# Optimization experiments

Measured on AMD Instinct MI355X. Metric: run time of the kernel, lower is better.

## Reference

```python
import jax, jax.numpy as jnp
import numpy as np

NUM_Q_HEADS = 32
NUM_KV_HEADS = 8
GROUP = NUM_Q_HEADS // NUM_KV_HEADS  # 4, matches hardcoded repeat_interleave(repeats=4)
HEAD_DIM = 128
ROPE_BASE = 10000.0


def _rope_cos_sin(seq_len, head_dim, dtype):
    # [S, D/2] angle tables for rotate-half RoPE
    inv_freq = 1.0 / (ROPE_BASE ** (jnp.arange(0, head_dim, 2, dtype=jnp.float32) / head_dim))
    ang = jnp.arange(seq_len, dtype=jnp.float32)[:, None] * inv_freq[None, :]
    return jnp.cos(ang).astype(dtype), jnp.sin(ang).astype(dtype)


def _apply_rope(x, cos, sin):
    # x: [B, S, H, D]; cos/sin: [S, D/2] broadcast over batch & heads
    x1, x2 = jnp.split(x, 2, axis=-1)
    c = cos[None, :, None, :]
    s = sin[None, :, None, :]
    return jnp.concatenate([x1 * c - x2 * s, x2 * c + x1 * s], axis=-1)


def setup_inputs() -> dict:
    key = jax.random.key(0)
    k1, k2, k3 = jax.random.split(key, 3)
    B, S, E = 2, 2048, 4096
    x = jax.random.normal(k1, (B, S, E), dtype=jnp.float32)
    w_in = jax.random.normal(k2, (6144, E), dtype=jnp.float32) * 0.02   # torch Linear weight [out, in]
    w_out = jax.random.normal(k3, (E, E), dtype=jnp.float32) * 0.02
    return {"x": x, "w_in": w_in, "w_out": w_out}


def reference(x, w_in, w_out):
    B, S, E = x.shape
    D = HEAD_DIM
    qkv = jnp.einsum('bse,fe->bsf', x, w_in)  # [B, S, 6144]
    parts = jnp.split(qkv, GROUP + 2, axis=-1)  # 6 equal chunks of width E//GROUP
    q = jnp.concatenate(parts[:GROUP], axis=-1).reshape(B, S, NUM_Q_HEADS, D)
    k = parts[GROUP].reshape(B, S, NUM_KV_HEADS, D)
    v = parts[GROUP + 1].reshape(B, S, NUM_KV_HEADS, D)

    cos, sin = _rope_cos_sin(S, D, x.dtype)
    q = _apply_rope(q, cos, sin)
    k = _apply_rope(k, cos, sin)

    # GQA without materializing repeated K/V: group q heads by kv head.
    # repeat_interleave(k, 4, dim=2) maps q head h -> kv head h // 4, i.e. q view [B,S,HKV,G,D]
    qg = q.reshape(B, S, NUM_KV_HEADS, GROUP, D)
    scale = 1.0 / jnp.sqrt(jnp.asarray(D, dtype=x.dtype))
    scores = jnp.einsum('bqhgd,bkhd->bhgqk', qg, k) * scale  # [B, HKV, G, S, S]
    causal = jnp.tril(jnp.ones((S, S), dtype=bool))
    scores = jnp.where(causal[None, None, None, :, :], scores, jnp.asarray(-1e30, dtype=scores.dtype))
    probs = jax.nn.softmax(scores, axis=-1)
    out = jnp.einsum('bhgqk,bkhd->bqhgd', probs, v)  # [B, S, HKV, G, D]
    out = out.reshape(B, S, E)
    return jnp.einsum('bse,fe->bsf', out, w_out)
```

## Files before the change

kernel.cpp:

```cpp
#include <hip/hip_runtime.h>
#include <hip/hip_bf16.h>
#include <stdint.h>

typedef unsigned short u16;
typedef __bf16 bf16x8 __attribute__((ext_vector_type(8)));
typedef u16 u16x8 __attribute__((ext_vector_type(8)));
typedef float f32x4 __attribute__((ext_vector_type(4)));
typedef float f32x16 __attribute__((ext_vector_type(16)));
typedef uint32_t u32x4 __attribute__((ext_vector_type(4)));

#define DEV __device__ __forceinline__
#define SBAR() asm volatile("s_barrier" ::: "memory")
#define SCHEDB() __builtin_amdgcn_sched_barrier(0)

DEV u16 f2bf(float f) {
  uint32_t u = __builtin_bit_cast(uint32_t, f);
  return (u16)((u + 0x7FFFu + ((u >> 16) & 1u)) >> 16);
}
DEV float bf2f(u16 h) { return __builtin_bit_cast(float, (uint32_t)h << 16); }

DEV void gload_lds16(const void* g, void* l) {
  __builtin_amdgcn_global_load_lds((const __attribute__((address_space(1))) uint32_t*)g,
                                   (__attribute__((address_space(3))) uint32_t*)l, 16, 0, 0);
}

DEV uint32_t cvtpk(float lo, float hi) {
  uint32_t r;
  asm("v_cvt_pk_bf16_f32 %0, %1, %2" : "=v"(r) : "v"(lo), "v"(hi));
  return r;
}
DEV void plswap(uint32_t& a, uint32_t& b) {
  asm("v_permlane32_swap_b32 %0, %1" : "+v"(a), "+v"(b));
}

DEV void cvt8(const float* __restrict__ in, u16* __restrict__ out, int i) {
  const float4* p = reinterpret_cast<const float4*>(in + i);
  float4 a = p[0], b = p[1];
  u16x8 o;
  o[0] = f2bf(a.x); o[1] = f2bf(a.y); o[2] = f2bf(a.z); o[3] = f2bf(a.w);
  o[4] = f2bf(b.x); o[5] = f2bf(b.y); o[6] = f2bf(b.z); o[7] = f2bf(b.w);
  *reinterpret_cast<u16x8*>(out + i) = o;
}

__global__ void prep_all(const float* __restrict__ x, const float* __restrict__ w_in,
                         const float* __restrict__ w_out, u16* __restrict__ xb,
                         u16* __restrict__ wib, u16* __restrict__ wob,
                         float* __restrict__ ct, float* __restrict__ st) {
  int b = blockIdx.x;
  if (b < 8192) {
    cvt8(x, xb, (b * 256 + threadIdx.x) * 8);
  } else if (b < 20480) {
    cvt8(w_in, wib, ((b - 8192) * 256 + threadIdx.x) * 8);
  } else if (b < 28672) {
    cvt8(w_out, wob, ((b - 20480) * 256 + threadIdx.x) * 8);
  } else {
    int i = (b - 28672) * 256 + threadIdx.x;
    int s = i >> 6, d = i & 63;
    float invf = powf(10000.0f, -(float)d * (1.0f / 64.0f));
    float ang = (float)s * invf;
    ct[i] = cosf(ang);
    st[i] = sinf(ang);
  }
}

__global__ void rope_and_vt(u16* __restrict__ qkv, const float* __restrict__ ct,
                            const float* __restrict__ st, u16* __restrict__ vtg) {
  const int tid = threadIdx.x;
  if (blockIdx.x < 5120) {
    int idx = blockIdx.x * 256 + tid;
    int grp = idx & 7;
    int head = (idx >> 3) % 40;
    int row = idx / 320;
    int s = row & 2047;
    size_t f0 = head < 32 ? (size_t)head * 128 : (size_t)4096 + (size_t)(head - 32) * 128;
    u16* p = qkv + (size_t)row * 6144 + f0 + grp * 8;
    u16x8 a = *reinterpret_cast<const u16x8*>(p);
    u16x8 b = *reinterpret_cast<const u16x8*>(p + 64);
    const float4* cp = reinterpret_cast<const float4*>(ct + s * 64 + grp * 8);
    const float4* sp = reinterpret_cast<const float4*>(st + s * 64 + grp * 8);
    float4 c0 = cp[0], c1 = cp[1], s0 = sp[0], s1 = sp[1];
    float cc[8] = {c0.x, c0.y, c0.z, c0.w, c1.x, c1.y, c1.z, c1.w};
    float ss[8] = {s0.x, s0.y, s0.z, s0.w, s1.x, s1.y, s1.z, s1.w};
    u16x8 o1, o2;
#pragma unroll
    for (int i = 0; i < 8; i++) {
      float x1 = bf2f(a[i]), x2 = bf2f(b[i]);
      o1[i] = f2bf(x1 * cc[i] - x2 * ss[i]);
      o2[i] = f2bf(x2 * cc[i] + x1 * ss[i]);
    }
    *reinterpret_cast<u16x8*>(p) = o1;
    *reinterpret_cast<u16x8*>(p + 64) = o2;
  } else {
    int id = blockIdx.x - 5120;
    int j = id & 31, kvh = (id >> 5) & 7, b = id >> 8;
    const size_t rowB = (size_t)b * 2048;
    u16* img = vtg + (size_t)id * 8192;
#pragma unroll
    for (int p = 0; p < 4; p++) {
      int lin = p * 256 + tid;
      int d = lin >> 3, c = lin & 7;
      const u16* src = qkv + (rowB + j * 64 + c * 8) * 6144 + 5120 + kvh * 128 + d;
      u16x8 v;
#pragma unroll
      for (int i = 0; i < 8; i++) v[i] = src[(size_t)i * 6144];
      *reinterpret_cast<u16x8*>(img + d * 64 + ((c ^ (d & 7)) << 3)) = v;
    }
  }
}

DEV void store_c(float* C, size_t idx, float v) { C[idx] = v; }
DEV void store_c(u16* C, size_t idx, float v) { C[idx] = f2bf(v); }

template <typename OutT>
__global__ __launch_bounds__(512, 2) void gemm256(const u16* __restrict__ A, const u16* __restrict__ B,
                                                  OutT* __restrict__ C, int M, int N, int K, int ldc) {
  __shared__ __align__(16) u16 lds[65536];
  char* LB = (char*)lds;
  const int tid = threadIdx.x;
  const int w = tid >> 6, lane = tid & 63;
  const int l15 = lane & 15, l4 = lane >> 4;
  const int wm = w >> 2, wn = w & 3;

  int nwg = gridDim.x;
  int q = nwg >> 3, rr = nwg & 7;
  int xcd = blockIdx.x & 7, idx = blockIdx.x >> 3;
  int sw = (xcd < rr ? xcd * (q + 1) : rr * (q + 1) + (xcd - rr) * q) + idx;
  int gxn = N >> 8;
  int by = sw / gxn, bx = sw - by * gxn;
  const int row0 = by << 8, col0 = bx << 8;
  const int NT = K >> 6;

  const int srow = w * 8 + (lane >> 3);
  const int sc16 = (lane & 7) ^ ((lane >> 3) & 7);
  const u16* gA = A + (size_t)(row0 + srow) * K + sc16 * 8;
  const u16* gB = B + (size_t)(col0 + srow) * K + sc16 * 8;

  const int fl = (l15 & 7) << 4;
  const int aoff = (wm * 128 + l15) * 128 + l4 * 16;
  const int boff = (wn * 64 + l15) * 128 + l4 * 16;

  f32x4 acc[8][4] = {};
  bf16x8 fA[4][2], fB0[2][2], fBc[2][2];

#define STAGE_A(kt, h, base)                                                      \
  {                                                                               \
    const u16* g_ = gA + (size_t)((h)*128) * K + (size_t)(kt)*64;                 \
    gload_lds16(g_, (base) + (h)*16384 + w * 1024);                               \
    gload_lds16(g_ + (size_t)64 * K, (base) + (h)*16384 + 8192 + w * 1024);       \
  }
#define STAGE_B(kt, h, base)                                                      \
  {                                                                               \
    const u16* g_ = gB + (size_t)((h)*128) * K + (size_t)(kt)*64;                 \
    gload_lds16(g_, (base) + (h)*16384 + w * 1024);                               \
    gload_lds16(g_ + (size_t)64 * K, (base) + (h)*16384 + 8192 + w * 1024);       \
  }
#define MFMA_Q(FB, MH, NH)                                                        \
  _Pragma("unroll") for (int kk = 0; kk < 2; kk++) {                              \
    _Pragma("unroll") for (int mf = 0; mf < 4; mf++) {                            \
      _Pragma("unroll") for (int nf = 0; nf < 2; nf++) {                          \
        acc[(MH)*4 + mf][(NH)*2 + nf] = __builtin_amdgcn_mfma_f32_16x16x32_bf16(  \
            fA[mf][kk], FB[nf][kk], acc[(MH)*4 + mf][(NH)*2 + nf], 0, 0, 0);      \
      }                                                                           \
    }                                                                             \
  }

  STAGE_A(0, 0, LB);
  STAGE_A(0, 1, LB);
  STAGE_B(0, 0, LB + 65536);
  STAGE_B(0, 1, LB + 65536);
  STAGE_A(1, 0, LB + 32768);
  STAGE_B(1, 0, LB + 98304);
  STAGE_B(1, 1, LB + 98304);
  asm volatile("s_waitcnt vmcnt(6)" ::: "memory");
  SBAR();

  for (int t = 0; t < NT; ++t) {
    char* ac = LB + (t & 1) * 32768;
    char* bc = LB + 65536 + (t & 1) * 32768;
    char* an = LB + ((t + 1) & 1) * 32768;

    if (t + 1 < NT) STAGE_A(t + 1, 1, an);

#pragma unroll
    for (int mf = 0; mf < 4; mf++)
#pragma unroll
      for (int kk = 0; kk < 2; kk++)
        fA[mf][kk] = *(const bf16x8*)(ac + ((aoff + mf * 2048 + kk * 64) ^ fl));
    SCHEDB();
#pragma unroll
    for (int nf = 0; nf < 2; nf++)
#pragma unroll
      for (int kk = 0; kk < 2; kk++)
        fB0[nf][kk] = *(const bf16x8*)(bc + ((boff + nf * 2048 + kk * 64) ^ fl));
    SCHEDB();
#pragma unroll
    for (int nf = 0; nf < 2; nf++)
#pragma unroll
      for (int kk = 0; kk < 2; kk++)
        fBc[nf][kk] = *(const bf16x8*)(bc + ((boff + (nf + 2) * 2048 + kk * 64) ^ fl));
    SCHEDB();

    asm volatile("s_waitcnt lgkmcnt(4)" ::: "memory");
    SCHEDB();
    __builtin_amdgcn_s_setprio(1);
    MFMA_Q(fB0, 0, 0);
    __builtin_amdgcn_s_setprio(0);

    asm volatile("s_waitcnt lgkmcnt(0)" ::: "memory");
    SCHEDB();
    __builtin_amdgcn_s_setprio(1);
    MFMA_Q(fBc, 0, 1);
    __builtin_amdgcn_s_setprio(0);

#pragma unroll
    for (int mf = 0; mf < 4; mf++)
#pragma unroll
      for (int kk = 0; kk < 2; kk++)
        fA[mf][kk] = *(const bf16x8*)(ac + ((aoff + (mf + 4) * 2048 + kk * 64) ^ fl));
    asm volatile("s_waitcnt lgkmcnt(0)" ::: "memory");
    SCHEDB();

    SBAR();
    if (t + 2 < NT) {
      STAGE_B(t + 2, 0, bc);
      STAGE_B(t + 2, 1, bc);
      STAGE_A(t + 2, 0, ac);
    }
    __builtin_amdgcn_s_setprio(1);
    MFMA_Q(fBc, 1, 1);
    MFMA_Q(fB0, 1, 0);
    __builtin_amdgcn_s_setprio(0);

    if (t + 2 < NT) {
      asm volatile("s_waitcnt vmcnt(6)" ::: "memory");
      SBAR();
    } else if (t + 1 < NT) {
      asm volatile("s_waitcnt vmcnt(0)" ::: "memory");
      SBAR();
    }
  }

#pragma unroll
  for (int mf = 0; mf < 8; mf++)
#pragma unroll
    for (int nf = 0; nf < 4; nf++)
#pragma unroll
      for (int r = 0; r < 4; r++) {
        size_t row = (size_t)row0 + wm * 128 + mf * 16 + l4 * 4 + r;
        size_t col = (size_t)col0 + wn * 64 + nf * 16 + l15;
        store_c(C, row * (size_t)ldc + col, acc[mf][nf][r]);
      }
#undef STAGE_A
#undef STAGE_B
#undef MFMA_Q
}

__global__ __launch_bounds__(512, 2) void gemm_bn128(const u16* __restrict__ A, const u16* __restrict__ B,
                                                     u16* __restrict__ C, int M, int N, int K, int ldc) {
  __shared__ __align__(16) u16 lds[49152];
  char* LB = (char*)lds;
  const int tid = threadIdx.x;
  const int w = tid >> 6, lane = tid & 63;
  const int l15 = lane & 15, l4 = lane >> 4;
  const int wm = w >> 2, wn = w & 3;

  int nwg = gridDim.x;
  int q = nwg >> 3, rr = nwg & 7;
  int xcd = blockIdx.x & 7, idx = blockIdx.x >> 3;
  int sw = (xcd < rr ? xcd * (q + 1) : rr * (q + 1) + (xcd - rr) * q) + idx;
  int gxn = N >> 7;
  int by = sw / gxn, bx = sw - by * gxn;
  const int row0 = by << 8, col0 = bx << 7;
  const int NT = K >> 6;

  const int srow = w * 8 + (lane >> 3);
  const int sc16 = (lane & 7) ^ ((lane >> 3) & 7);
  const u16* gA = A + (size_t)(row0 + srow) * K + sc16 * 8;
  const u16* gB = B + (size_t)(col0 + srow) * K + sc16 * 8;

  const int fl = (l15 & 7) << 4;
  const int aoff = (wm * 128 + l15) * 128 + l4 * 16;
  const int boff = (wn * 32 + l15) * 128 + l4 * 16;

  f32x4 acc[8][2] = {};
  bf16x8 fA[4][2], fB[2][2];

#define STAGE_A(kt, h, base)                                                      \
  {                                                                               \
    const u16* g_ = gA + (size_t)((h)*128) * K + (size_t)(kt)*64;                 \
    gload_lds16(g_, (base) + (h)*16384 + w * 1024);                               \
    gload_lds16(g_ + (size_t)64 * K, (base) + (h)*16384 + 8192 + w * 1024);       \
  }
#define STAGE_B(kt, base)                                                         \
  {                                                                               \
    const u16* g_ = gB + (size_t)(kt)*64;                                         \
    gload_lds16(g_, (base) + w * 1024);                                           \
    gload_lds16(g_ + (size_t)64 * K, (base) + 8192 + w * 1024);                   \
  }

  STAGE_A(0, 0, LB);
  STAGE_A(0, 1, LB);
  STAGE_B(0, LB + 65536);
  STAGE_A(1, 0, LB + 32768);
  STAGE_B(1, LB + 65536 + 16384);
  asm volatile("s_waitcnt vmcnt(4)" ::: "memory");
  SBAR();

  for (int t = 0; t < NT; ++t) {
    char* ac = LB + (t & 1) * 32768;
    char* bc = LB + 65536 + (t & 1) * 16384;
    char* an = LB + ((t + 1) & 1) * 32768;

    if (t + 1 < NT) STAGE_A(t + 1, 1, an);

#pragma unroll
    for (int mf = 0; mf < 4; mf++)
#pragma unroll
      for (int kk = 0; kk < 2; kk++)
        fA[mf][kk] = *(const bf16x8*)(ac + ((aoff + mf * 2048 + kk * 64) ^ fl));
#pragma unroll
    for (int nf = 0; nf < 2; nf++)
#pragma unroll
      for (int kk = 0; kk < 2; kk++)
        fB[nf][kk] = *(const bf16x8*)(bc + ((boff + nf * 2048 + kk * 64) ^ fl));
    SCHEDB();
    asm volatile("s_waitcnt lgkmcnt(0)" ::: "memory");
    SCHEDB();
    __builtin_amdgcn_s_setprio(1);
#pragma unroll
    for (int kk = 0; kk < 2; kk++)
#pragma unroll
      for (int mf = 0; mf < 4; mf++)
#pragma unroll
        for (int nf = 0; nf < 2; nf++)
          acc[mf][nf] = __builtin_amdgcn_mfma_f32_16x16x32_bf16(fA[mf][kk], fB[nf][kk], acc[mf][nf], 0, 0, 0);
    __builtin_amdgcn_s_setprio(0);

#pragma unroll
    for (int mf = 0; mf < 4; mf++)
#pragma unroll
      for (int kk = 0; kk < 2; kk++)
        fA[mf][kk] = *(const bf16x8*)(ac + ((aoff + (mf + 4) * 2048 + kk * 64) ^ fl));
    asm volatile("s_waitcnt lgkmcnt(0)" ::: "memory");
    SCHEDB();

    SBAR();
    if (t + 2 < NT) {
      STAGE_A(t + 2, 0, ac);
      STAGE_B(t + 2, bc);
    }
    __builtin_amdgcn_s_setprio(1);
#pragma unroll
    for (int kk = 0; kk < 2; kk++)
#pragma unroll
      for (int mf = 0; mf < 4; mf++)
#pragma unroll
        for (int nf = 0; nf < 2; nf++)
          acc[mf + 4][nf] = __builtin_amdgcn_mfma_f32_16x16x32_bf16(fA[mf][kk], fB[nf][kk], acc[mf + 4][nf], 0, 0, 0);
    __builtin_amdgcn_s_setprio(0);

    if (t + 2 < NT) {
      asm volatile("s_waitcnt vmcnt(4)" ::: "memory");
      SBAR();
    } else if (t + 1 < NT) {
      asm volatile("s_waitcnt vmcnt(0)" ::: "memory");
      SBAR();
    }
  }

#pragma unroll
  for (int mf = 0; mf < 8; mf++)
#pragma unroll
    for (int nf = 0; nf < 2; nf++)
#pragma unroll
      for (int r = 0; r < 4; r++) {
        size_t row = (size_t)row0 + wm * 128 + mf * 16 + l4 * 4 + r;
        size_t col = (size_t)col0 + wn * 32 + nf * 16 + l15;
        C[row * (size_t)ldc + col] = f2bf(acc[mf][nf][r]);
      }
#undef STAGE_A
#undef STAGE_B
}

__global__ __launch_bounds__(256, 2) void attn_fwd(const u16* __restrict__ qkv,
                                                   const u16* __restrict__ vtg,
                                                   u16* __restrict__ out) {
  constexpr int S = 2048, F = 6144, E = 4096;
  __shared__ __align__(16) u16 Kt[2 * 8192];
  __shared__ __align__(16) u16 Vt[2 * 8192];

  const int tid = threadIdx.x;
  const int w = tid >> 6, lane = tid & 63;
  const int l31 = lane & 31, hi = lane >> 5;
  const int pair = blockIdx.x;
  const int b = blockIdx.y >> 5, h = blockIdx.y & 31, kvh = h >> 2;
  const size_t rowB = (size_t)b * S;
  const float sc = 0.08838834764831845f * 1.4426950408889634f;
  const int sgn = tid >> 4, sgc = tid & 15;
  const size_t vtb = (size_t)(b * 8 + kvh) * 32 * 8192;

  auto stage = [&](int j, int buf) {
    char* kd = ((char*)Kt) + buf * 16384 + w * 1024;
    char* vd = ((char*)Vt) + buf * 16384 + w * 1024;
    const u16* vs = vtg + vtb + (size_t)j * 8192 + tid * 8;
#pragma unroll
    for (int p = 0; p < 4; p++) {
      int n = p * 16 + sgn;
      const u16* g = qkv + (rowB + j * 64 + n) * F + 4096 + kvh * 128 + (sgc ^ (n & 7)) * 8;
      gload_lds16(g, kd + p * 4096);
      gload_lds16(vs + p * 2048, vd + p * 4096);
    }
  };

  for (int half = 0; half < 2; ++half) {
    const int t = half ? 15 - pair : pair;
    const int nt = 2 * t + 2;
    const int r0 = t * 128;
    const int qg = r0 + w * 32 + l31;

    bf16x8 qf[8];
    {
      const u16* qp = qkv + (rowB + qg) * F + h * 128 + hi * 8;
#pragma unroll
      for (int ds = 0; ds < 8; ds++) qf[ds] = *reinterpret_cast<const bf16x8*>(qp + ds * 16);
    }

    f32x16 acco[4] = {};
    float m = -1e30f, l = 0.f;

    stage(0, 0);
    __syncthreads();

    for (int j = 0; j < nt; ++j) {
      const int cur = j & 1;
      if (j + 1 < nt) stage(j + 1, cur ^ 1);

      const char* kbase = ((const char*)Kt) + cur * 16384;
      f32x16 s0 = {}, s1 = {};
      __builtin_amdgcn_s_setprio(1);
#pragma unroll
      for (int ds = 0; ds < 8; ds++) {
        int ch = ((2 * ds + hi) ^ (l31 & 7)) << 4;
        bf16x8 k0 = *reinterpret_cast<const bf16x8*>(kbase + l31 * 256 + ch);
        bf16x8 k1 = *reinterpret_cast<const bf16x8*>(kbase + (32 + l31) * 256 + ch);
        s0 = __builtin_amdgcn_mfma_f32_32x32x16_bf16(k0, qf[ds], s0, 0, 0, 0);
        s1 = __builtin_amdgcn_mfma_f32_32x32x16_bf16(k1, qf[ds], s1, 0, 0, 0);
      }
      __builtin_amdgcn_s_setprio(0);

      f32x16 px0, px1;
      if (j >= 2 * t) {
#pragma unroll
        for (int rg = 0; rg < 16; rg++) {
          int kv0 = j * 64 + (rg & 3) + 8 * (rg >> 2) + 4 * hi;
          px0[rg] = (kv0 > qg) ? -1e30f : s0[rg] * sc;
          px1[rg] = (kv0 + 32 > qg) ? -1e30f : s1[rg] * sc;
        }
      } else {
#pragma unroll
        for (int rg = 0; rg < 16; rg++) {
          px0[rg] = s0[rg] * sc;
          px1[rg] = s1[rg] * sc;
        }
      }

      float mt[8];
#pragma unroll
      for (int i = 0; i < 8; i++)
        mt[i] = fmaxf(fmaxf(px0[i], px0[i + 8]), fmaxf(px1[i], px1[i + 8]));
#pragma unroll
      for (int stp = 4; stp; stp >>= 1)
#pragma unroll
        for (int i = 0; i < stp; i++) mt[i] = fmaxf(mt[i], mt[i + stp]);
      float pm = fmaxf(mt[0], __shfl_xor(mt[0], 32));

      if (__any(pm > m + 8.0f)) {
        float mn = fmaxf(m, pm);
        float fr = exp2f(m - mn);
        m = mn;
        l *= fr;
#pragma unroll
        for (int rg = 0; rg < 16; rg++) {
          int qrow = (rg & 3) + 8 * (rg >> 2) + 4 * hi;
          float frq = __builtin_bit_cast(
              float, __builtin_amdgcn_ds_bpermute(qrow << 2, __builtin_bit_cast(int, fr)));
          acco[0][rg] *= frq;
          acco[1][rg] *= frq;
          acco[2][rg] *= frq;
          acco[3][rg] *= frq;
        }
      }

#pragma unroll
      for (int rg = 0; rg < 16; rg++) {
        px0[rg] = exp2f(px0[rg] - m);
        px1[rg] = exp2f(px1[rg] - m);
      }
      float at[8];
#pragma unroll
      for (int i = 0; i < 8; i++)
        at[i] = (px0[i] + px0[i + 8]) + (px1[i] + px1[i + 8]);
#pragma unroll
      for (int stp = 4; stp; stp >>= 1)
#pragma unroll
        for (int i = 0; i < stp; i++) at[i] += at[i + stp];
      l += at[0] + __shfl_xor(at[0], 32);

      const char* vbase = ((const char*)Vt) + cur * 16384;
      __builtin_amdgcn_s_setprio(1);
#define PV_STEP(PH, SS)                                                               \
  {                                                                                   \
    uint32_t X0 = cvtpk(PH[((SS)&1) * 8 + 0], PH[((SS)&1) * 8 + 1]);                  \
    uint32_t Y0 = cvtpk(PH[((SS)&1) * 8 + 4], PH[((SS)&1) * 8 + 5]);                  \
    uint32_t X1 = cvtpk(PH[((SS)&1) * 8 + 2], PH[((SS)&1) * 8 + 3]);                  \
    uint32_t Y1 = cvtpk(PH[((SS)&1) * 8 + 6], PH[((SS)&1) * 8 + 7]);                  \
    plswap(X0, Y0);                                                                   \
    plswap(X1, Y1);                                                                   \
    u32x4 pw = {X0, X1, Y0, Y1};                                                      \
    bf16x8 pa = __builtin_bit_cast(bf16x8, pw);                                       \
    _Pragma("unroll") for (int df = 0; df < 4; df++) {                                \
      bf16x8 vf = *reinterpret_cast<const bf16x8*>(                                   \
          vbase + (32 * df + l31) * 128 + (((2 * (SS) + hi) ^ (l31 & 7)) << 4));      \
      acco[df] = __builtin_amdgcn_mfma_f32_32x32x16_bf16(pa, vf, acco[df], 0, 0, 0);  \
    }                                                                                 \
  }
      PV_STEP(px0, 0)
      PV_STEP(px0, 1)
      PV_STEP(px1, 2)
      PV_STEP(px1, 3)
#undef PV_STEP
      __builtin_amdgcn_s_setprio(0);

      __syncthreads();
    }

    float linv = 1.f / l;
#pragma unroll
    for (int rg = 0; rg < 16; rg++) {
      int qrow = (rg & 3) + 8 * (rg >> 2) + 4 * hi;
      float lv = __builtin_bit_cast(
          float, __builtin_amdgcn_ds_bpermute(qrow << 2, __builtin_bit_cast(int, linv)));
      size_t row = rowB + r0 + w * 32 + qrow;
      u16* op = out + row * E + h * 128 + l31;
#pragma unroll
      for (int df = 0; df < 4; df++) op[df * 32] = f2bf(acco[df][rg] * lv);
    }
  }
}

extern "C" void kernel_launch(void* const* d_in, const int* in_sizes, int n_in,
                              void* d_out, int out_size, void* d_ws, size_t ws_size,
                              hipStream_t stream) {
  const float* x = (const float*)d_in[0];
  const float* w_in = (const float*)d_in[1];
  const float* w_out = (const float*)d_in[2];
  float* out = (float*)d_out;
  char* ws = (char*)d_ws;

  u16* xb = (u16*)(ws);
  u16* wib = (u16*)(ws + 33554432ull);
  u16* wob = (u16*)(ws + 83886080ull);
  u16* qkvb = (u16*)(ws + 117440512ull);
  float* ct = (float*)(ws + 167772160ull);
  float* st = ct + 2048 * 64;
  u16* attnb = xb;
  u16* vtg = wib;

  prep_all<<<29184, 256, 0, stream>>>(x, w_in, w_out, xb, wib, wob, ct, st);
  gemm256<u16><<<256, 512, 0, stream>>>(xb, wib, qkvb, 4096, 4096, 4096, 6144);
  gemm_bn128<<<256, 512, 0, stream>>>(xb, wib + (size_t)4096 * 4096, qkvb + 4096, 4096, 2048, 4096, 6144);
  rope_and_vt<<<5632, 256, 0, stream>>>(qkvb, ct, st, vtg);
  attn_fwd<<<dim3(8, 64), 256, 0, stream>>>(qkvb, vtg, attnb);
  gemm256<float><<<256, 512, 0, stream>>>(attnb, wob, out, 4096, 4096, 4096, 4096);
}
```

Before: 494.4 us.

## Restructure gemm256 to K=32 tiles with triple-buffered LDS pipeline

Rewrites the main 256x256 GEMM loop to stage K-slices of 32 instead of 64, using three 32KB LDS buffers (96KB total instead of 128KB) and prefetching two tiles ahead with a single barrier per iteration. All fragments for a tile are loaded at once, then 32 MFMAs are issued. This removes the split mid-iteration barrier and half-tile staging, at the cost of twice as many loop iterations and less MFMA work per LDS wait. Two unrelated renames in gemm_bn128 avoid a name clash.

```diff
diff --git a/kernel.cpp b/kernel.cpp
--- a/kernel.cpp
+++ b/kernel.cpp
@@ -12,6 +12,7 @@
 #define DEV __device__ __forceinline__
 #define SBAR() asm volatile("s_barrier" ::: "memory")
 #define SCHEDB() __builtin_amdgcn_sched_barrier(0)
+#define LGKM0() do { asm volatile("s_waitcnt lgkmcnt(0)" ::: "memory"); SCHEDB(); } while (0)
 
 DEV u16 f2bf(float f) {
   uint32_t u = __builtin_bit_cast(uint32_t, f);
@@ -114,7 +115,7 @@
 template <typename OutT>
 __global__ __launch_bounds__(512, 2) void gemm256(const u16* __restrict__ A, const u16* __restrict__ B,
                                                   OutT* __restrict__ C, int M, int N, int K, int ldc) {
-  __shared__ __align__(16) u16 lds[65536];
+  __shared__ __align__(16) u16 lds[49152];
   char* LB = (char*)lds;
   const int tid = threadIdx.x;
   const int w = tid >> 6, lane = tid & 63;
@@ -128,116 +129,67 @@
   int gxn = N >> 8;
   int by = sw / gxn, bx = sw - by * gxn;
   const int row0 = by << 8, col0 = bx << 8;
-  const int NT = K >> 6;
-
-  const int srow = w * 8 + (lane >> 3);
-  const int sc16 = (lane & 7) ^ ((lane >> 3) & 7);
-  const u16* gA = A + (size_t)(row0 + srow) * K + sc16 * 8;
-  const u16* gB = B + (size_t)(col0 + srow) * K + sc16 * 8;
-
-  const int fl = (l15 & 7) << 4;
-  const int aoff = (wm * 128 + l15) * 128 + l4 * 16;
-  const int boff = (wn * 64 + l15) * 128 + l4 * 16;
+  const int NT = K >> 5;
+
+  const int srow = w * 16 + (lane >> 2);
+  const int sc = (lane & 3) ^ ((lane >> 3) & 3);
+  const u16* gA = A + (size_t)(row0 + srow) * K + sc * 8;
+  const u16* gB = B + (size_t)(col0 + srow) * K + sc * 8;
+
+  const int fl = ((l15 >> 1) & 3) << 4;
+  const int aoff = (wm * 128 + l15) * 64 + l4 * 16;
+  const int boff = (wn * 64 + l15) * 64 + l4 * 16;
 
   f32x4 acc[8][4] = {};
-  bf16x8 fA[4][2], fB0[2][2], fBc[2][2];
-
-#define STAGE_A(kt, h, base)                                                      \
-  {                                                                               \
-    const u16* g_ = gA + (size_t)((h)*128) * K + (size_t)(kt)*64;                 \
-    gload_lds16(g_, (base) + (h)*16384 + w * 1024);                               \
-    gload_lds16(g_ + (size_t)64 * K, (base) + (h)*16384 + 8192 + w * 1024);       \
-  }
-#define STAGE_B(kt, h, base)                                                      \
-  {                                                                               \
-    const u16* g_ = gB + (size_t)((h)*128) * K + (size_t)(kt)*64;                 \
-    gload_lds16(g_, (base) + (h)*16384 + w * 1024);                               \
-    gload_lds16(g_ + (size_t)64 * K, (base) + (h)*16384 + 8192 + w * 1024);       \
-  }
-#define MFMA_Q(FB, MH, NH)                                                        \
-  _Pragma("unroll") for (int kk = 0; kk < 2; kk++) {                              \
-    _Pragma("unroll") for (int mf = 0; mf < 4; mf++) {                            \
-      _Pragma("unroll") for (int nf = 0; nf < 2; nf++) {                          \
-        acc[(MH)*4 + mf][(NH)*2 + nf] = __builtin_amdgcn_mfma_f32_16x16x32_bf16(  \
-            fA[mf][kk], FB[nf][kk], acc[(MH)*4 + mf][(NH)*2 + nf], 0, 0, 0);      \
-      }                                                                           \
-    }                                                                             \
-  }
-
-  STAGE_A(0, 0, LB);
-  STAGE_A(0, 1, LB);
-  STAGE_B(0, 0, LB + 65536);
-  STAGE_B(0, 1, LB + 65536);
-  STAGE_A(1, 0, LB + 32768);
-  STAGE_B(1, 0, LB + 98304);
-  STAGE_B(1, 1, LB + 98304);
-  asm volatile("s_waitcnt vmcnt(6)" ::: "memory");
+  bf16x8 fA[8], fB[4];
+
+#define STAGE_A(kt, h, bb) \
+  gload_lds16(gA + (size_t)((h)*128) * K + (size_t)(kt)*32, (bb) + (h)*8192 + w * 1024);
+#define STAGE_B(kt, h, bb) \
+  gload_lds16(gB + (size_t)((h)*128) * K + (size_t)(kt)*32, (bb) + 16384 + (h)*8192 + w * 1024);
+#define STAGE_TILE(kt, bb)  \
+  {                         \
+    STAGE_A(kt, 0, bb);     \
+    STAGE_A(kt, 1, bb);     \
+    STAGE_B(kt, 0, bb);     \
+    STAGE_B(kt, 1, bb);     \
+  }
+
+  STAGE_TILE(0, LB);
+  STAGE_TILE(1, LB + 32768);
+  asm volatile("s_waitcnt vmcnt(4)" ::: "memory");
   SBAR();
 
+  int bc = 0, bs = 2;
   for (int t = 0; t < NT; ++t) {
-    char* ac = LB + (t & 1) * 32768;
-    char* bc = LB + 65536 + (t & 1) * 32768;
-    char* an = LB + ((t + 1) & 1) * 32768;
-
-    if (t + 1 < NT) STAGE_A(t + 1, 1, an);
-
-#pragma unroll
-    for (int mf = 0; mf < 4; mf++)
-#pragma unroll
-      for (int kk = 0; kk < 2; kk++)
-        fA[mf][kk] = *(const bf16x8*)(ac + ((aoff + mf * 2048 + kk * 64) ^ fl));
-    SCHEDB();
-#pragma unroll
-    for (int nf = 0; nf < 2; nf++)
-#pragma unroll
-      for (int kk = 0; kk < 2; kk++)
-        fB0[nf][kk] = *(const bf16x8*)(bc + ((boff + nf * 2048 + kk * 64) ^ fl));
-    SCHEDB();
-#pragma unroll
-    for (int nf = 0; nf < 2; nf++)
-#pragma unroll
-      for (int kk = 0; kk < 2; kk++)
-        fBc[nf][kk] = *(const bf16x8*)(bc + ((boff + (nf + 2) * 2048 + kk * 64) ^ fl));
-    SCHEDB();
-
-    asm volatile("s_waitcnt lgkmcnt(4)" ::: "memory");
-    SCHEDB();
+    char* cb = LB + bc * 32768;
+    if (t + 2 < NT) STAGE_TILE(t + 2, LB + bs * 32768);
+
+#pragma unroll
+    for (int mf = 0; mf < 8; mf++)
+      fA[mf] = *(const bf16x8*)(cb + ((aoff + mf * 1024) ^ fl));
+#pragma unroll
+    for (int nf = 0; nf < 4; nf++)
+      fB[nf] = *(const bf16x8*)(cb + 16384 + ((boff + nf * 1024) ^ fl));
+    LGKM0();
+
     __builtin_amdgcn_s_setprio(1);
-    MFMA_Q(fB0, 0, 0);
+#pragma unroll
+    for (int mf = 0; mf < 8; mf++)
+#pragma unroll
+      for (int nf = 0; nf < 4; nf++)
+        acc[mf][nf] = __builtin_amdgcn_mfma_f32_16x16x32_bf16(fA[mf], fB[nf], acc[mf][nf], 0, 0, 0);
     __builtin_amdgcn_s_setprio(0);
 
-    asm volatile("s_waitcnt lgkmcnt(0)" ::: "memory");
-    SCHEDB();
-    __builtin_amdgcn_s_setprio(1);
-    MFMA_Q(fBc, 0, 1);
-    __builtin_amdgcn_s_setprio(0);
-
-#pragma unroll
-    for (int mf = 0; mf < 4; mf++)
-#pragma unroll
-      for (int kk = 0; kk < 2; kk++)
-        fA[mf][kk] = *(const bf16x8*)(ac + ((aoff + (mf + 4) * 2048 + kk * 64) ^ fl));
-    asm volatile("s_waitcnt lgkmcnt(0)" ::: "memory");
-    SCHEDB();
-
-    SBAR();
     if (t + 2 < NT) {
-      STAGE_B(t + 2, 0, bc);
-      STAGE_B(t + 2, 1, bc);
-      STAGE_A(t + 2, 0, ac);
-    }
-    __builtin_amdgcn_s_setprio(1);
-    MFMA_Q(fBc, 1, 1);
-    MFMA_Q(fB0, 1, 0);
-    __builtin_amdgcn_s_setprio(0);
-
-    if (t + 2 < NT) {
-      asm volatile("s_waitcnt vmcnt(6)" ::: "memory");
+      asm volatile("s_waitcnt vmcnt(4)" ::: "memory");
       SBAR();
     } else if (t + 1 < NT) {
       asm volatile("s_waitcnt vmcnt(0)" ::: "memory");
       SBAR();
     }
+    bc = bc == 2 ? 0 : bc + 1;
+    bs = bs == 2 ? 0 : bs + 1;
   }
 
 #pragma unroll
@@ -252,7 +204,7 @@
       }
 #undef STAGE_A
 #undef STAGE_B
-#undef MFMA_Q
+#undef STAGE_TILE
 }
 
 __global__ __launch_bounds__(512, 2) void gemm_bn128(const u16* __restrict__ A, const u16* __restrict__ B,
@@ -308,7 +260,7 @@
 
   for (int t = 0; t < NT; ++t) {
     char* ac = LB + (t & 1) * 32768;
-    char* bc = LB + 65536 + (t & 1) * 16384;
+    char* bcc = LB + 65536 + (t & 1) * 16384;
     char* an = LB + ((t + 1) & 1) * 32768;
 
     if (t + 1 < NT) STAGE_A(t + 1, 1, an);
@@ -322,7 +274,7 @@
     for (int nf = 0; nf < 2; nf++)
 #pragma unroll
       for (int kk = 0; kk < 2; kk++)
-        fB[nf][kk] = *(const bf16x8*)(bc + ((boff + nf * 2048 + kk * 64) ^ fl));
+        fB[nf][kk] = *(const bf16x8*)(bcc + ((boff + nf * 2048 + kk * 64) ^ fl));
     SCHEDB();
     asm volatile("s_waitcnt lgkmcnt(0)" ::: "memory");
     SCHEDB();
@@ -347,7 +299,7 @@
     SBAR();
     if (t + 2 < NT) {
       STAGE_A(t + 2, 0, ac);
-      STAGE_B(t + 2, bc);
+      STAGE_B(t + 2, bcc);
     }
     __builtin_amdgcn_s_setprio(1);
 #pragma unroll
```

New measurement: 515.0 us. 1.04x slower.
